# Performance work log

Measured on AMD Instinct MI355X. Metric: run time of the kernel, lower is better.

The kernel has to match this reference:

```python
import jax, jax.numpy as jnp
import numpy as np

B, L, D = 8, 2048, 512
H, P = 8, 4
C = D // H  # dim_per_head


def setup_inputs() -> dict:
    key = jax.random.key(0)
    ks = jax.random.split(key, 11)
    sc = lambda k, shape, s=0.02: jax.random.normal(k, shape, jnp.float32) * s
    return dict(
        query=jax.random.normal(ks[0], (B, L, D), jnp.float32),
        key_in=jax.random.normal(ks[1], (B, L, D), jnp.float32),
        value=jax.random.normal(ks[2], (B, L, D), jnp.float32),
        W_v=sc(ks[3], (D, D)), b_v=jnp.zeros((D,), jnp.float32),
        W_off=sc(ks[4], (D, H * P * 2), 0.01), b_off=sc(ks[5], (H * P * 2,), 0.2),
        W_aw=sc(ks[6], (D, H * P), 0.01), b_aw=jnp.zeros((H * P,), jnp.float32),
        W_out=sc(ks[7], (D, D)), b_out=jnp.zeros((D,), jnp.float32),
    )


def reference(query, key_in, value, W_v, b_v, W_off, b_off, W_aw, b_aw, W_out, b_out):
    # value projection
    v = value @ W_v + b_v                                        # (B,L,D)
    # sampling offsets and attention weights from the query
    off = (query @ W_off + b_off).reshape(B, L, H, P, 2)         # (B,L,H,P,2)
    aw = jax.nn.softmax((query @ W_aw + b_aw).reshape(B, L, H, P), axis=-1)
    # reference point for query i is (x=linspace[0]=0, y=linspace[i]) because
    # the torch code slices reference_points[:, :, :, :1, :]
    ref_y = jnp.linspace(0.0, 1.0, L, dtype=jnp.float32)
    loc_x = jnp.clip(off[..., 0], 0.0, 1.0)                      # ref_x = 0
    loc_y = jnp.clip(off[..., 1] + ref_y[None, :, None, None], 0.0, 1.0)
    # grid_sample, align_corners=False, input (BH, C, 1, L)
    ix = ((loc_x + 1.0) * L - 1.0) * 0.5                         # width coord in [ (L-1)/2, L-0.5 ]
    iy = loc_y * 0.5                                             # ((y+1)*1 - 1)/2
    ix0 = jnp.floor(ix)
    fx = ix - ix0
    iy0 = jnp.floor(iy)
    fy = iy - iy0
    # height dim has size 1: row iy0 valid iff ==0, row iy0+1 valid iff ==0 (zero padding)
    ywt = (1.0 - fy) * (iy0 == 0.0).astype(jnp.float32) + fy * ((iy0 + 1.0) == 0.0).astype(jnp.float32)
    i0 = ix0.astype(jnp.int32)
    i1 = i0 + 1

    perm = lambda a: a.transpose(0, 2, 1, 3)                     # (B,L,H,P) -> (B,H,L,P)
    i0p, i1p = perm(i0), perm(i1)
    vh = v.reshape(B, L, H, C).transpose(0, 2, 1, 3)             # (B,H,L,C)

    gather = jax.vmap(jax.vmap(lambda vm, ii: vm[ii]))           # (L,C),(L,P) -> (L,P,C)
    m0 = ((i0p >= 0) & (i0p < L)).astype(jnp.float32)[..., None]
    m1 = ((i1p >= 0) & (i1p < L)).astype(jnp.float32)[..., None]
    g0 = gather(vh, jnp.clip(i0p, 0, L - 1)) * m0                # (B,H,L,P,C)
    g1 = gather(vh, jnp.clip(i1p, 0, L - 1)) * m1

    fxp = perm(fx)[..., None]
    ywtp = perm(ywt)[..., None]
    samp = ywtp * ((1.0 - fxp) * g0 + fxp * g1)                  # (B,H,L,P,C)
    out = (samp * perm(aw)[..., None]).sum(axis=3)               # (B,H,L,C)
    out = out.transpose(0, 2, 1, 3).reshape(B, L, D)
    return out @ W_out + b_out
```

## Files before the change

### kernel.cpp

```cpp
#include <hip/hip_runtime.h>
#include <stdint.h>

#define M_ROWS 16384

using short8  = __attribute__((ext_vector_type(8))) short;
using floatx4 = __attribute__((ext_vector_type(4))) float;

__device__ __forceinline__ unsigned short f2bf(float f) {
  union { float f; unsigned u; } v; v.f = f;
  unsigned r = v.u + 0x7fffu + ((v.u >> 16) & 1u);
  return (unsigned short)(r >> 16);
}
__device__ __forceinline__ float bf2f(unsigned short u) {
  union { unsigned u; float f; } v; v.u = ((unsigned)u) << 16; return v.f;
}

__device__ __forceinline__ void load_lds16(const unsigned short* g, unsigned short* l) {
  __builtin_amdgcn_global_load_lds(
      (const __attribute__((address_space(1))) unsigned int*)g,
      (__attribute__((address_space(3))) unsigned int*)l, 16, 0, 0);
}

__device__ __forceinline__ void store_val(float* p, float v) { *p = v; }
__device__ __forceinline__ void store_val(unsigned short* p, float v) { *p = f2bf(v); }


__global__ __launch_bounds__(256) void conv_bf16(const float* __restrict__ src,
                                                 unsigned short* __restrict__ dst, int n4) {
  int i = blockIdx.x * 256 + threadIdx.x;
  if (i >= n4) return;
  float4 v = ((const float4*)src)[i];
  ushort4 o;
  o.x = f2bf(v.x); o.y = f2bf(v.y); o.z = f2bf(v.z); o.w = f2bf(v.w);
  ((ushort4*)dst)[i] = o;
}

__global__ __launch_bounds__(256) void transpose_bf16(const float* __restrict__ src,
                                                      unsigned short* __restrict__ dst) {
  int idx = blockIdx.x * 256 + threadIdx.x;
  int n = idx >> 9, k = idx & 511;
  dst[idx] = f2bf(src[(k << 9) + n]);
}

__global__ __launch_bounds__(256) void buildcat(const float* __restrict__ Woff,
                                                const float* __restrict__ Waw,
                                                const float* __restrict__ boff,
                                                const float* __restrict__ baw,
                                                float* __restrict__ Wcat,
                                                float* __restrict__ bcat) {
  int idx = blockIdx.x * 256 + threadIdx.x;
  if (idx < 512 * 96) {
    int k = idx / 96, n = idx - k * 96;
    Wcat[idx] = (n < 64) ? Woff[(k << 6) + n] : Waw[(k << 5) + (n - 64)];
  }
  if (idx < 96) bcat[idx] = (idx < 64) ? boff[idx] : baw[idx - 64];
}

template <typename OutT>
__global__ __launch_bounds__(256) void gemm_bt(const unsigned short* __restrict__ A,
                                               const unsigned short* __restrict__ Bt,
                                               const float* __restrict__ bias,
                                               OutT* __restrict__ C, int N, int K) {
  __shared__ __align__(16) unsigned short lA[128 * 32];
  __shared__ __align__(16) unsigned short lB[128 * 32];
  int tid  = threadIdx.x;
  int lane = tid & 63, wv = tid >> 6;
  int wm = wv & 1, wn = wv >> 1;
  int lrow = lane & 15, quad = lane >> 4;
  int rowBlk = blockIdx.y * 128, colBlk = blockIdx.x * 128;

  const unsigned short* Ab = A + (size_t)rowBlk * K;
  const unsigned short* Bb = Bt + (size_t)colBlk * K;
  int r0 = tid >> 2;
  int c0 = (tid & 3) << 3;

  floatx4 acc[4][4];
#pragma unroll
  for (int i = 0; i < 4; i++)
#pragma unroll
    for (int j = 0; j < 4; j++) acc[i][j] = (floatx4){0.f, 0.f, 0.f, 0.f};

  for (int k0 = 0; k0 < K; k0 += 32) {
    load_lds16(Ab + (size_t)r0 * K + k0 + c0,        lA + tid * 8);
    load_lds16(Ab + (size_t)(r0 + 64) * K + k0 + c0, lA + 2048 + tid * 8);
    load_lds16(Bb + (size_t)r0 * K + k0 + c0,        lB + tid * 8);
    load_lds16(Bb + (size_t)(r0 + 64) * K + k0 + c0, lB + 2048 + tid * 8);
    __syncthreads();

    short8 a[4], b[4];
#pragma unroll
    for (int mi = 0; mi < 4; mi++)
      a[mi] = *(const short8*)&lA[(wm * 64 + mi * 16 + lrow) * 32 + quad * 8];
#pragma unroll
    for (int ni = 0; ni < 4; ni++)
      b[ni] = *(const short8*)&lB[(wn * 64 + ni * 16 + lrow) * 32 + quad * 8];
#pragma unroll
    for (int mi = 0; mi < 4; mi++)
#pragma unroll
      for (int ni = 0; ni < 4; ni++)
        acc[mi][ni] = __builtin_amdgcn_mfma_f32_16x16x32_bf16(a[mi], b[ni], acc[mi][ni], 0, 0, 0);
    __syncthreads();
  }

#pragma unroll
  for (int ni = 0; ni < 4; ni++) {
    int col = colBlk + wn * 64 + ni * 16 + lrow;
    float bv = bias[col];
#pragma unroll
    for (int mi = 0; mi < 4; mi++) {
      int row = rowBlk + wm * 64 + mi * 16 + quad * 4;
#pragma unroll
      for (int r = 0; r < 4; r++)
        store_val(&C[(size_t)(row + r) * N + col], acc[mi][ni][r] + bv);
    }
  }
}

__global__ __launch_bounds__(256) void offaw_gemm(const float* __restrict__ Q,
                                                  const float* __restrict__ Wcat,
                                                  const float* __restrict__ bcat,
                                                  float* __restrict__ p0,
                                                  float* __restrict__ p1) {
  __shared__ float lA[64 * 16];
  __shared__ float lB[16 * 96];
  int tid = threadIdx.x;
  int khalf = blockIdx.x;
  int row0 = blockIdx.y * 64;
  int tx = tid & 15, ty = tid >> 4;
  int ar = tid >> 2, ac = (tid & 3) << 2;

  float acc[4][6];
#pragma unroll
  for (int i = 0; i < 4; i++)
#pragma unroll
    for (int j = 0; j < 6; j++) acc[i][j] = 0.f;

  int kbeg = khalf * 256;
  for (int k0 = kbeg; k0 < kbeg + 256; k0 += 16) {
    *(float4*)&lA[ar * 16 + ac] = *(const float4*)&Q[(size_t)(row0 + ar) * 512 + k0 + ac];
#pragma unroll
    for (int j = 0; j < 6; j++) {
      int e = tid + j * 256;
      lB[e] = Wcat[(size_t)k0 * 96 + e];
    }
    __syncthreads();
#pragma unroll
    for (int kk = 0; kk < 16; kk++) {
      float a[4], b[6];
#pragma unroll
      for (int i = 0; i < 4; i++) a[i] = lA[(ty + (i << 4)) * 16 + kk];
#pragma unroll
      for (int j = 0; j < 6; j++) b[j] = lB[kk * 96 + tx + (j << 4)];
#pragma unroll
      for (int i = 0; i < 4; i++)
#pragma unroll
        for (int j = 0; j < 6; j++) acc[i][j] += a[i] * b[j];
    }
    __syncthreads();
  }

  float* outp = (khalf == 0) ? p0 : p1;
#pragma unroll
  for (int i = 0; i < 4; i++) {
    int r = row0 + ty + (i << 4);
#pragma unroll
    for (int j = 0; j < 6; j++) {
      int c = tx + (j << 4);
      float v = acc[i][j];
      if (khalf == 0) v += bcat[c];
      outp[(size_t)r * 96 + c] = v;
    }
  }
}

__global__ __launch_bounds__(256) void sample_kernel(const float* __restrict__ p0,
                                                     const float* __restrict__ p1,
                                                     const unsigned short* __restrict__ v,
                                                     unsigned short* __restrict__ attn) {
  int row = blockIdx.x;
  int b = row >> 11, l = row & 2047;
  __shared__ float s_w0[32], s_w1[32];
  __shared__ int s_i0[32], s_i1[32];
  int tid = threadIdx.x;

  if (tid < 32) {
    int base = row * 96;
    float lg = p0[base + 64 + tid] + p1[base + 64 + tid];
    float mx = fmaxf(lg, __shfl_xor(lg, 1));
    mx = fmaxf(mx, __shfl_xor(mx, 2));
    float e = __expf(lg - mx);
    float s = e + __shfl_xor(e, 1);
    s = s + __shfl_xor(s, 2);
    float aw = e / s;

    float ox = p0[base + 2 * tid] + p1[base + 2 * tid];
    float oy = p0[base + 2 * tid + 1] + p1[base + 2 * tid + 1];
    float refy = (float)l * (1.0f / 2047.0f);
    float lx = fminf(fmaxf(ox, 0.0f), 1.0f);
    float ly = fminf(fmaxf(oy + refy, 0.0f), 1.0f);
    float ix = ((lx + 1.0f) * 2048.0f - 1.0f) * 0.5f;
    float ywt = 1.0f - ly * 0.5f;
    float ix0 = floorf(ix);
    float fx = ix - ix0;
    int i0 = (int)ix0;
    int i1 = i0 + 1;
    s_w0[tid] = aw * ywt * (1.0f - fx);
    s_w1[tid] = (i1 < 2048) ? (aw * ywt * fx) : 0.0f;
    s_i0[tid] = i0;
    s_i1[tid] = (i1 < 2048) ? i1 : 2047;
  }
  __syncthreads();

  const unsigned short* vb = v + ((size_t)(b << 11)) * 512;
  int c = tid & 63;
#pragma unroll
  for (int hh = 0; hh < 2; hh++) {
    int h = (tid >> 6) + (hh << 2);
    const unsigned short* vhc = vb + h * 64 + c;
    float acc = 0.0f;
#pragma unroll
    for (int p = 0; p < 4; p++) {
      int t = (h << 2) + p;
      acc += s_w0[t] * bf2f(vhc[(size_t)s_i0[t] << 9]) +
             s_w1[t] * bf2f(vhc[(size_t)s_i1[t] << 9]);
    }
    attn[(size_t)row * 512 + h * 64 + c] = f2bf(acc);
  }
}

extern "C" void kernel_launch(void* const* d_in, const int* in_sizes, int n_in,
                              void* d_out, int out_size, void* d_ws, size_t ws_size,
                              hipStream_t stream) {
  (void)in_sizes; (void)n_in; (void)out_size; (void)ws_size;
  const float* query = (const float*)d_in[0];
  const float* value = (const float*)d_in[2];
  const float* W_v   = (const float*)d_in[3];
  const float* b_v   = (const float*)d_in[4];
  const float* W_off = (const float*)d_in[5];
  const float* b_off = (const float*)d_in[6];
  const float* W_aw  = (const float*)d_in[7];
  const float* b_aw  = (const float*)d_in[8];
  const float* W_out = (const float*)d_in[9];
  const float* b_out = (const float*)d_in[10];
  float* out = (float*)d_out;

  char* ws = (char*)d_ws;
  const size_t MB = 1ull << 20;
  unsigned short* val_bf = (unsigned short*)(ws);
  unsigned short* attn   = val_bf;
  unsigned short* v_bf   = (unsigned short*)(ws + 16 * MB);
  float* offp0           = (float*)(ws + 32 * MB);
  float* offp1           = (float*)(ws + 38 * MB);
  unsigned short* Wv_t   = (unsigned short*)(ws + 44 * MB);
  unsigned short* Wo_t   = (unsigned short*)(ws + 44 * MB + 524288);
  float* Wcat            = (float*)(ws + 45 * MB);
  float* bcat            = (float*)(ws + 45 * MB + 196608);

  conv_bf16<<<8192, 256, 0, stream>>>(value, val_bf, 2097152);
  transpose_bf16<<<1024, 256, 0, stream>>>(W_v, Wv_t);
  transpose_bf16<<<1024, 256, 0, stream>>>(W_out, Wo_t);
  buildcat<<<192, 256, 0, stream>>>(W_off, W_aw, b_off, b_aw, Wcat, bcat);

  gemm_bt<unsigned short><<<dim3(4, 128), 256, 0, stream>>>(val_bf, Wv_t, b_v, v_bf, 512, 512);
  offaw_gemm<<<dim3(2, 256), 256, 0, stream>>>(query, Wcat, bcat, offp0, offp1);
  sample_kernel<<<16384, 256, 0, stream>>>(offp0, offp1, v_bf, attn);
  gemm_bt<float><<<dim3(4, 128), 256, 0, stream>>>(attn, Wo_t, b_out, out, 512, 512);
}
```

Before: 232.8 us.

## Compute offset/attention-weight projection with split-bf16 MFMA instead of FP32 FMA

Replaces the scalar FP32 tiled GEMM for the query offset/weight projection with a bf16 MFMA kernel. It uses a three-term hi/lo split (Ahi*Bhi, Ahi*Blo, Alo*Bhi) to approximate FP32 precision. Each term writes a separate partial buffer, and the sample kernel sums the three. The aim is to move this K=512 GEMM onto matrix cores. The cost is three passes over the query, on-the-fly bf16 conversion, and more partial-buffer traffic.

Result: no change. 231.1 us (-0.7%).

```diff
diff --git a/kernel.cpp b/kernel.cpp
--- a/kernel.cpp
+++ b/kernel.cpp
@@ -2,6 +2,7 @@
 #include <stdint.h>
 
 #define M_ROWS 16384
+#define PSZF (16384 * 96)
 
 using short8  = __attribute__((ext_vector_type(8))) short;
 using floatx4 = __attribute__((ext_vector_type(4))) float;
@@ -46,12 +47,16 @@
                                                 const float* __restrict__ Waw,
                                                 const float* __restrict__ boff,
                                                 const float* __restrict__ baw,
-                                                float* __restrict__ Wcat,
+                                                unsigned short* __restrict__ Bhi,
+                                                unsigned short* __restrict__ Blo,
                                                 float* __restrict__ bcat) {
   int idx = blockIdx.x * 256 + threadIdx.x;
-  if (idx < 512 * 96) {
-    int k = idx / 96, n = idx - k * 96;
-    Wcat[idx] = (n < 64) ? Woff[(k << 6) + n] : Waw[(k << 5) + (n - 64)];
+  if (idx < 96 * 512) {
+    int n = idx >> 9, k = idx & 511;
+    float w = (n < 64) ? Woff[(k << 6) + n] : Waw[(k << 5) + (n - 64)];
+    unsigned short hi = f2bf(w);
+    Bhi[idx] = hi;
+    Blo[idx] = f2bf(w - bf2f(hi));
   }
   if (idx < 96) bcat[idx] = (idx < 64) ? boff[idx] : baw[idx - 64];
 }
@@ -116,65 +121,83 @@
   }
 }
 
-__global__ __launch_bounds__(256) void offaw_gemm(const float* __restrict__ Q,
-                                                  const float* __restrict__ Wcat,
+__global__ __launch_bounds__(128) void offaw_mfma(const float* __restrict__ Q,
+                                                  const unsigned short* __restrict__ Bhi,
+                                                  const unsigned short* __restrict__ Blo,
                                                   const float* __restrict__ bcat,
-                                                  float* __restrict__ p0,
-                                                  float* __restrict__ p1) {
-  __shared__ float lA[64 * 16];
-  __shared__ float lB[16 * 96];
+                                                  float* __restrict__ P) {
+  __shared__ __align__(16) unsigned short lA[64 * 32];
+  __shared__ __align__(16) unsigned short lB[96 * 32];
+  int seg = blockIdx.x;
+  int row0 = blockIdx.y * 64;
   int tid = threadIdx.x;
-  int khalf = blockIdx.x;
-  int row0 = blockIdx.y * 64;
-  int tx = tid & 15, ty = tid >> 4;
-  int ar = tid >> 2, ac = (tid & 3) << 2;
-
-  float acc[4][6];
+  int lane = tid & 63, wn = tid >> 6;
+  int lrow = lane & 15, quad = lane >> 4;
+  const unsigned short* Bt = (seg == 1) ? Blo : Bhi;
+  bool wantlo = (seg == 2);
+  float* out = P + (size_t)seg * PSZF;
+
+  int ar = tid >> 1;
+  int ach = (tid & 1) << 4;
+
+  floatx4 acc[4][3];
 #pragma unroll
   for (int i = 0; i < 4; i++)
 #pragma unroll
-    for (int j = 0; j < 6; j++) acc[i][j] = 0.f;
-
-  int kbeg = khalf * 256;
-  for (int k0 = kbeg; k0 < kbeg + 256; k0 += 16) {
-    *(float4*)&lA[ar * 16 + ac] = *(const float4*)&Q[(size_t)(row0 + ar) * 512 + k0 + ac];
-#pragma unroll
-    for (int j = 0; j < 6; j++) {
-      int e = tid + j * 256;
-      lB[e] = Wcat[(size_t)k0 * 96 + e];
-    }
-    __syncthreads();
-#pragma unroll
-    for (int kk = 0; kk < 16; kk++) {
-      float a[4], b[6];
-#pragma unroll
-      for (int i = 0; i < 4; i++) a[i] = lA[(ty + (i << 4)) * 16 + kk];
-#pragma unroll
-      for (int j = 0; j < 6; j++) b[j] = lB[kk * 96 + tx + (j << 4)];
-#pragma unroll
-      for (int i = 0; i < 4; i++)
-#pragma unroll
-        for (int j = 0; j < 6; j++) acc[i][j] += a[i] * b[j];
-    }
-    __syncthreads();
-  }
-
-  float* outp = (khalf == 0) ? p0 : p1;
-#pragma unroll
-  for (int i = 0; i < 4; i++) {
-    int r = row0 + ty + (i << 4);
-#pragma unroll
-    for (int j = 0; j < 6; j++) {
-      int c = tx + (j << 4);
-      float v = acc[i][j];
-      if (khalf == 0) v += bcat[c];
-      outp[(size_t)r * 96 + c] = v;
-    }
-  }
-}
-
-__global__ __launch_bounds__(256) void sample_kernel(const float* __restrict__ p0,
-                                                     const float* __restrict__ p1,
+    for (int j = 0; j < 3; j++) acc[i][j] = (floatx4){0.f, 0.f, 0.f, 0.f};
+
+  const float* qrow = Q + (size_t)(row0 + ar) * 512 + ach;
+
+  for (int k0 = 0; k0 < 512; k0 += 32) {
+#pragma unroll
+    for (int j = 0; j < 4; j++) {
+      float4 v = *(const float4*)(qrow + k0 + j * 4);
+      if (wantlo) {
+        v.x -= bf2f(f2bf(v.x)); v.y -= bf2f(f2bf(v.y));
+        v.z -= bf2f(f2bf(v.z)); v.w -= bf2f(f2bf(v.w));
+      }
+      ushort4 o;
+      o.x = f2bf(v.x); o.y = f2bf(v.y); o.z = f2bf(v.z); o.w = f2bf(v.w);
+      *(ushort4*)&lA[ar * 32 + ach + j * 4] = o;
+    }
+#pragma unroll
+    for (int j = 0; j < 3; j++) {
+      int e = tid + j * 128;
+      int n = e >> 2, c = (e & 3) << 3;
+      load_lds16(Bt + (size_t)n * 512 + k0 + c, lB + e * 8);
+    }
+    __syncthreads();
+
+    short8 a[4], b[3];
+#pragma unroll
+    for (int mi = 0; mi < 4; mi++)
+      a[mi] = *(const short8*)&lA[(mi * 16 + lrow) * 32 + quad * 8];
+#pragma unroll
+    for (int ni = 0; ni < 3; ni++)
+      b[ni] = *(const short8*)&lB[(wn * 48 + ni * 16 + lrow) * 32 + quad * 8];
+#pragma unroll
+    for (int mi = 0; mi < 4; mi++)
+#pragma unroll
+      for (int ni = 0; ni < 3; ni++)
+        acc[mi][ni] = __builtin_amdgcn_mfma_f32_16x16x32_bf16(a[mi], b[ni], acc[mi][ni], 0, 0, 0);
+    __syncthreads();
+  }
+
+#pragma unroll
+  for (int ni = 0; ni < 3; ni++) {
+    int col = wn * 48 + ni * 16 + lrow;
+    float bv = (seg == 0) ? bcat[col] : 0.0f;
+#pragma unroll
+    for (int mi = 0; mi < 4; mi++) {
+      int row = row0 + mi * 16 + quad * 4;
+#pragma unroll
+      for (int r = 0; r < 4; r++)
+        out[(size_t)(row + r) * 96 + col] = acc[mi][ni][r] + bv;
+    }
+  }
+}
+
+__global__ __launch_bounds__(256) void sample_kernel(const float* __restrict__ P,
                                                      const unsigned short* __restrict__ v,
                                                      unsigned short* __restrict__ attn) {
   int row = blockIdx.x;
@@ -185,7 +208,7 @@
 
   if (tid < 32) {
     int base = row * 96;
-    float lg = p0[base + 64 + tid] + p1[base + 64 + tid];
+    float lg = P[base + 64 + tid] + P[PSZF + base + 64 + tid] + P[2 * PSZF + base + 64 + tid];
     float mx = fmaxf(lg, __shfl_xor(lg, 1));
     mx = fmaxf(mx, __shfl_xor(mx, 2));
     float e = __expf(lg - mx);
@@ -193,8 +216,8 @@
     s = s + __shfl_xor(s, 2);
     float aw = e / s;
 
-    float ox = p0[base + 2 * tid] + p1[base + 2 * tid];
-    float oy = p0[base + 2 * tid + 1] + p1[base + 2 * tid + 1];
+    float ox = P[base + 2 * tid] + P[PSZF + base + 2 * tid] + P[2 * PSZF + base + 2 * tid];
+    float oy = P[base + 2 * tid + 1] + P[PSZF + base + 2 * tid + 1] + P[2 * PSZF + base + 2 * tid + 1];
     float refy = (float)l * (1.0f / 2047.0f);
     float lx = fminf(fmaxf(ox, 0.0f), 1.0f);
     float ly = fminf(fmaxf(oy + refy, 0.0f), 1.0f);
@@ -249,20 +272,20 @@
   unsigned short* val_bf = (unsigned short*)(ws);
   unsigned short* attn   = val_bf;
   unsigned short* v_bf   = (unsigned short*)(ws + 16 * MB);
-  float* offp0           = (float*)(ws + 32 * MB);
-  float* offp1           = (float*)(ws + 38 * MB);
-  unsigned short* Wv_t   = (unsigned short*)(ws + 44 * MB);
-  unsigned short* Wo_t   = (unsigned short*)(ws + 44 * MB + 524288);
-  float* Wcat            = (float*)(ws + 45 * MB);
-  float* bcat            = (float*)(ws + 45 * MB + 196608);
+  float* offP            = (float*)(ws + 32 * MB);
+  unsigned short* Wv_t   = (unsigned short*)(ws + 50 * MB);
+  unsigned short* Wo_t   = (unsigned short*)(ws + 50 * MB + 524288);
+  unsigned short* Bhi    = (unsigned short*)(ws + 51 * MB);
+  unsigned short* Blo    = (unsigned short*)(ws + 51 * MB + 98304);
+  float* bcat            = (float*)(ws + 51 * MB + 196608);
 
   conv_bf16<<<8192, 256, 0, stream>>>(value, val_bf, 2097152);
   transpose_bf16<<<1024, 256, 0, stream>>>(W_v, Wv_t);
   transpose_bf16<<<1024, 256, 0, stream>>>(W_out, Wo_t);
-  buildcat<<<192, 256, 0, stream>>>(W_off, W_aw, b_off, b_aw, Wcat, bcat);
+  buildcat<<<192, 256, 0, stream>>>(W_off, W_aw, b_off, b_aw, Bhi, Blo, bcat);
 
   gemm_bt<unsigned short><<<dim3(4, 128), 256, 0, stream>>>(val_bf, Wv_t, b_v, v_bf, 512, 512);
-  offaw_gemm<<<dim3(2, 256), 256, 0, stream>>>(query, Wcat, bcat, offp0, offp1);
-  sample_kernel<<<16384, 256, 0, stream>>>(offp0, offp1, v_bf, attn);
+  offaw_mfma<<<dim3(3, 256), 128, 0, stream>>>(query, Bhi, Blo, bcat, offP);
+  sample_kernel<<<16384, 256, 0, stream>>>(offP, v_bf, attn);
   gemm_bt<float><<<dim3(4, 128), 256, 0, stream>>>(attn, Wo_t, b_out, out, 512, 512);
 }
```
